# Performance work log

Measured on AMD Instinct MI355X. Metric: run time of the kernel, lower is better.

## Reference

```python
import jax, jax.numpy as jnp
import numpy as np

B, C, H, W = 4, 128, 64, 64
CQ = C // 8  # query/key channels = 16


def setup_inputs() -> dict:
    key = jax.random.key(0)
    ks = jax.random.split(key, 8)
    s = 0.05
    return {
        "x": jax.random.normal(ks[0], (B, C, H, W), jnp.float32),
        "wq": jax.random.normal(ks[1], (CQ, C), jnp.float32) * s,
        "bq": jax.random.normal(ks[2], (CQ,), jnp.float32) * s,
        "wk": jax.random.normal(ks[3], (CQ, C), jnp.float32) * s,
        "bk": jax.random.normal(ks[4], (CQ,), jnp.float32) * s,
        "wv": jax.random.normal(ks[5], (C, C), jnp.float32) * s,
        "bv": jax.random.normal(ks[6], (C,), jnp.float32) * s,
        # original inits gamma to 0; use small nonzero so attention path is exercised
        "gamma": jax.random.normal(ks[7], (1,), jnp.float32) * 0.1,
    }


def reference(x, wq, bq, wk, bk, wv, bv, gamma):
    b, c, h, w = x.shape
    n = h * w
    xf = x.reshape(b, c, n)  # [B, C, N]
    # 1x1 convs are per-position linear maps over channels
    q = jnp.einsum("qc,bcn->bnq", wq, xf) + bq            # [B, N, Cq]
    k = jnp.einsum("qc,bcn->bqn", wk, xf) + bk[:, None]   # [B, Cq, N]
    v = jnp.einsum("oc,bcn->bon", wv, xf) + bv[:, None]   # [B, C, N]
    # unscaled scores, softmax over keys (last dim), as in the original
    attn = jax.nn.softmax(jnp.einsum("bnq,bqm->bnm", q, k), axis=-1)  # [B, N, N]
    # out = value @ attention^T : out[b,c,n] = sum_m v[b,c,m] * attn[b,n,m]
    out = jnp.einsum("bom,bnm->bon", v, attn)             # [B, C, N]
    return gamma[0] * out.reshape(b, c, h, w) + x
```

## Files before the change

kernel.cpp:

```cpp
#include <hip/hip_runtime.h>
#include <hip/hip_bf16.h>

typedef float f32x4  __attribute__((ext_vector_type(4)));
typedef float f32x16 __attribute__((ext_vector_type(16)));
typedef short s16x8  __attribute__((ext_vector_type(8)));
typedef unsigned int u32;

#define NB 4
#define NC 128
#define NNPOS 4096
#define KSP 6
#define LOG2E 1.44269504088896f

__device__ __forceinline__ short bf16s(float x) {
    __hip_bfloat16 h = __float2bfloat16(x);
    return *reinterpret_cast<short*>(&h);
}
__device__ __forceinline__ int packbf2(float lo, float hi) {
    __hip_bfloat162 t = __float22bfloat162_rn(float2{lo, hi});
    return *reinterpret_cast<int*>(&t);
}
__device__ __forceinline__ float bf2f(unsigned short u) {
    unsigned int v = ((unsigned int)u) << 16;
    return *reinterpret_cast<float*>(&v);
}
__device__ __forceinline__ float exp2fast(float x) {
    return __builtin_amdgcn_exp2f(x);
}
__device__ __forceinline__ void gload_lds16(const short* g, short* l) {
    __builtin_amdgcn_global_load_lds(
        (const __attribute__((address_space(1))) u32*)g,
        (__attribute__((address_space(3))) u32*)l, 16, 0, 0);
}

__global__ __launch_bounds__(256) void qkv_kernel(
    const float* __restrict__ x,
    const float* __restrict__ wq, const float* __restrict__ bq,
    const float* __restrict__ wk, const float* __restrict__ bk,
    const float* __restrict__ wv, const float* __restrict__ bv,
    short* __restrict__ qb, short* __restrict__ kb, short* __restrict__ vt)
{
    const int n0  = blockIdx.x * 32;
    const int b   = blockIdx.y;
    const int tid = threadIdx.x;
    const int w = tid >> 6, lane = tid & 63, quad = lane >> 4, nn = lane & 15;

    __shared__ __align__(16) short xsT[32 * 136];
    __shared__ __align__(16) short vstage[4096];

    #pragma unroll
    for (int p = 0; p < 4; ++p) {
        int idx = tid + p * 256;
        int cc = idx >> 3, n4 = (idx & 7) * 4;
        f32x4 xv = *(const f32x4*)&x[((size_t)(b * NC + cc)) * NNPOS + n0 + n4];
        #pragma unroll
        for (int j = 0; j < 4; ++j)
            xsT[(n4 + j) * 136 + cc] = bf16s(xv[j]);
    }

    s16x8 af[3][4];
    bool  live[3];
    f32x4 biasv[3];
    #pragma unroll
    for (int t = 0; t < 3; ++t) {
        int rid = 3 * w + t;
        int R   = rid * 16;
        const float* wsrc = nullptr; const float* bsrc = nullptr; int row0 = 0;
        float scale = 1.0f;
        if (rid < 8)        { wsrc = wv; bsrc = bv; row0 = R; }
        else if (rid == 8)  { wsrc = wq; bsrc = bq; row0 = 0; scale = LOG2E; }
        else if (rid == 10) { wsrc = wk; bsrc = bk; row0 = 0; }
        live[t] = (wsrc != nullptr);
        #pragma unroll
        for (int r = 0; r < 4; ++r)
            biasv[t][r] = live[t] ? scale * bsrc[row0 + quad * 4 + r] : 0.0f;
        if (live[t]) {
            #pragma unroll
            for (int ks = 0; ks < 4; ++ks) {
                const float* src = wsrc + (size_t)(row0 + nn) * NC + ks * 32 + quad * 8;
                f32x4 wa = *(const f32x4*)src;
                f32x4 wb = *(const f32x4*)(src + 4);
                s16x8 f;
                #pragma unroll
                for (int j = 0; j < 4; ++j) {
                    f[j]     = bf16s(scale * wa[j]);
                    f[j + 4] = bf16s(scale * wb[j]);
                }
                af[t][ks] = f;
            }
        }
    }
    __syncthreads();

    f32x4 acc[3][2];
    #pragma unroll
    for (int t = 0; t < 3; ++t)
        #pragma unroll
        for (int nt = 0; nt < 2; ++nt)
            acc[t][nt] = biasv[t];

    #pragma unroll
    for (int nt = 0; nt < 2; ++nt) {
        s16x8 bf[4];
        #pragma unroll
        for (int ks = 0; ks < 4; ++ks)
            bf[ks] = *(const s16x8*)&xsT[(nt * 16 + nn) * 136 + ks * 32 + quad * 8];
        #pragma unroll
        for (int t = 0; t < 3; ++t)
            if (live[t])
                #pragma unroll
                for (int ks = 0; ks < 4; ++ks)
                    acc[t][nt] = __builtin_amdgcn_mfma_f32_16x16x32_bf16(af[t][ks], bf[ks], acc[t][nt], 0, 0, 0);
    }

    const int slot = (nn & 3) | ((nn & 4) << 1) | ((nn & 8) >> 1);

    #pragma unroll
    for (int t = 0; t < 3; ++t) {
        if (!live[t]) continue;
        const int rid = 3 * w + t;
        #pragma unroll
        for (int nt = 0; nt < 2; ++nt) {
            if (rid < 8) {
                #pragma unroll
                for (int r = 0; r < 4; ++r) {
                    int row = rid * 16 + quad * 4 + r;
                    vstage[(((nt << 2) | (row >> 5)) << 9) +
                           ((slot >> 3) << 8) + ((row & 31) << 3) + (slot & 7)]
                        = bf16s(acc[t][nt][r]);
                }
            } else {
                short4 pk;
                pk.x = bf16s(acc[t][nt][0]);
                pk.y = bf16s(acc[t][nt][1]);
                pk.z = bf16s(acc[t][nt][2]);
                pk.w = bf16s(acc[t][nt][3]);
                int n = n0 + nt * 16 + nn;
                short* dst = (rid == 8 ? qb : kb) +
                             ((size_t)(b * NNPOS) + n) * 16 + quad * 4;
                *reinterpret_cast<short4*>(dst) = pk;
            }
        }
    }
    __syncthreads();

    {
        short* vdst = vt + ((size_t)(b * 256) + (n0 >> 4)) * 2048;
        #pragma unroll
        for (int p = 0; p < 2; ++p) {
            int off = (tid + p * 256) * 8;
            *(s16x8*)&vdst[off] = *(const s16x8*)&vstage[off];
        }
    }
}

__global__ __launch_bounds__(256, 3) void attn_kernel(
    const short* __restrict__ qb, const short* __restrict__ kb,
    const short* __restrict__ vt,
    unsigned short* __restrict__ Ow, float* __restrict__ lw)
{
    const int s   = blockIdx.x;
    const int b   = blockIdx.z;
    const int tid = threadIdx.x;
    const int w = tid >> 6, lane = tid & 63, h = lane >> 5, c31 = lane & 31;

    const int q0 = (blockIdx.y * 4 + w) * 32;

    __shared__ __align__(16) short vlds[2][8192];

    s16x8 bq = *(const s16x8*)(qb + ((size_t)(b * NNPOS) + q0 + c31) * 16 + h * 8);

    f32x16 acc[4];
    #pragma unroll
    for (int ct = 0; ct < 4; ++ct)
        #pragma unroll
        for (int r = 0; r < 16; ++r) acc[ct][r] = 0.0f;
    float lp0 = 0.f, lp1 = 0.f;

    const short* kbp = kb + (size_t)(b * NNPOS) * 16;
    const int nit    = (s < 4) ? 11 : 10;
    const int mbase  = (s < 4) ? s * 704 : 2816 + (s - 4) * 640;
    const short* vtile = vt + (size_t)b * (NC * NNPOS) + ((size_t)(mbase >> 4) << 11);

    f32x16 z;
    #pragma unroll
    for (int r = 0; r < 16; ++r) z[r] = 0.0f;

    #pragma unroll
    for (int j = 0; j < 4; ++j)
        gload_lds16(vtile + (tid << 3) + (j << 11),
                    &vlds[0][0] + (tid << 3) + (j << 11));
    int m0 = mbase;
    s16x8 ak0 = *(const s16x8*)(kbp + (size_t)(m0      + c31) * 16 + h * 8);
    s16x8 ak1 = *(const s16x8*)(kbp + (size_t)(m0 + 32 + c31) * 16 + h * 8);
    __syncthreads();

    int buf = 0;
    for (int it = 0; it < nit; ++it) {
        if (it + 1 < nit) {
            const short* src = vtile + (((size_t)(it + 1)) << 13);
            short* dst = &vlds[buf ^ 1][0];
            #pragma unroll
            for (int j = 0; j < 4; ++j)
                gload_lds16(src + (tid << 3) + (j << 11),
                            dst + (tid << 3) + (j << 11));
        }

        f32x16 s0 = __builtin_amdgcn_mfma_f32_32x32x16_bf16(ak0, bq, z, 0, 0, 0);
        f32x16 s1 = __builtin_amdgcn_mfma_f32_32x32x16_bf16(ak1, bq, z, 0, 0, 0);

        if (it + 1 < nit) {
            m0 += 64;
            ak0 = *(const s16x8*)(kbp + (size_t)(m0      + c31) * 16 + h * 8);
            ak1 = *(const s16x8*)(kbp + (size_t)(m0 + 32 + c31) * 16 + h * 8);
        }

        s16x8 pa[4];
        #pragma unroll
        for (int p = 0; p < 4; ++p) {
            const f32x16& sv = (p < 2) ? s0 : s1;
            const int off = (p & 1) * 8;
            union { int i[4]; s16x8 v; } u;
            #pragma unroll
            for (int j = 0; j < 4; ++j) {
                float p0 = exp2fast(sv[off + 2 * j]);
                float p1 = exp2fast(sv[off + 2 * j + 1]);
                if (j & 1) lp1 += p0 + p1; else lp0 += p0 + p1;
                u.i[j] = packbf2(p0, p1);
            }
            pa[p] = u.v;
        }

        const short* vb = &vlds[buf][0];
        #pragma unroll
        for (int p = 0; p < 4; ++p)
            #pragma unroll
            for (int ct = 0; ct < 4; ++ct) {
                s16x8 vf = *(const s16x8*)&vb[((p * 4 + ct) << 9) + (lane << 3)];
                acc[ct] = __builtin_amdgcn_mfma_f32_32x32x16_bf16(
                    pa[p], vf, acc[ct], 0, 0, 0);
            }

        __syncthreads();
        buf ^= 1;
    }

    float lp = lp0 + lp1;
    lp += __shfl_xor(lp, 32, 64);
    if (lane < 32)
        lw[((size_t)(b * KSP + s)) * NNPOS + q0 + c31] = lp;

    #pragma unroll
    for (int ct = 0; ct < 4; ++ct)
        #pragma unroll
        for (int r = 0; r < 16; ++r) {
            int q = q0 + (r & 3) + 8 * (r >> 2) + 4 * h;
            Ow[(((size_t)(b * KSP + s)) * NNPOS + q) * NC + ct * 32 + c31] =
                (unsigned short)bf16s(acc[ct][r]);
        }
}

__global__ __launch_bounds__(256) void combine_kernel(
    const unsigned short* __restrict__ Ow, const float* __restrict__ lw,
    const float* __restrict__ x, const float* __restrict__ gamma,
    float* __restrict__ out)
{
    const int n0  = blockIdx.x * 64;
    const int b   = blockIdx.y;
    const int tid = threadIdx.x;

    __shared__ float ot[128 * 65 + 64];
    float* lsum = ot + 128 * 65;

    if (tid < 64) {
        float sl = 0.f;
        #pragma unroll
        for (int sI = 0; sI < KSP; ++sI)
            sl += lw[((size_t)(b * KSP + sI)) * NNPOS + n0 + tid];
        lsum[tid] = 1.0f / sl;
    }
    __syncthreads();

    #pragma unroll
    for (int p = 0; p < 4; ++p) {
        int e = tid + p * 256;
        int co = e & 15, n = e >> 4;
        float a[8] = {0.f, 0.f, 0.f, 0.f, 0.f, 0.f, 0.f, 0.f};
        #pragma unroll
        for (int sI = 0; sI < KSP; ++sI) {
            const unsigned short* src = Ow +
                (((size_t)(b * KSP + sI)) * NNPOS + n0 + n) * NC + co * 8;
            union { s16x8 v; unsigned short us[8]; } u;
            u.v = *(const s16x8*)src;
            #pragma unroll
            for (int j = 0; j < 8; ++j) a[j] += bf2f(u.us[j]);
        }
        float inv = lsum[n];
        #pragma unroll
        for (int j = 0; j < 8; ++j)
            ot[(co * 8 + j) * 65 + n] = a[j] * inv;
    }
    __syncthreads();

    const float g = gamma[0];
    #pragma unroll
    for (int p = 0; p < 8; ++p) {
        int e = tid + p * 256;
        int nq = e & 15, c = e >> 4;
        size_t a = ((size_t)(b * NC + c)) * NNPOS + n0 + nq * 4;
        float4 xv = *(const float4*)&x[a];
        float4 o;
        o.x = g * ot[c * 65 + nq * 4]     + xv.x;
        o.y = g * ot[c * 65 + nq * 4 + 1] + xv.y;
        o.z = g * ot[c * 65 + nq * 4 + 2] + xv.z;
        o.w = g * ot[c * 65 + nq * 4 + 3] + xv.w;
        *(float4*)&out[a] = o;
    }
}

extern "C" void kernel_launch(void* const* d_in, const int* in_sizes, int n_in,
                              void* d_out, int out_size, void* d_ws, size_t ws_size,
                              hipStream_t stream) {
    const float* x     = (const float*)d_in[0];
    const float* wq    = (const float*)d_in[1];
    const float* bq    = (const float*)d_in[2];
    const float* wk    = (const float*)d_in[3];
    const float* bk    = (const float*)d_in[4];
    const float* wv    = (const float*)d_in[5];
    const float* bv    = (const float*)d_in[6];
    const float* gamma = (const float*)d_in[7];
    float* out = (float*)d_out;

    short* qb = (short*)d_ws;
    short* kb = qb + (size_t)NB * NNPOS * 16;
    short* vt = kb + (size_t)NB * NNPOS * 16;
    unsigned short* Ow = (unsigned short*)(vt + (size_t)NB * NC * NNPOS);
    float* lw = (float*)(Ow + (size_t)NB * KSP * NNPOS * NC);

    qkv_kernel<<<dim3(128, NB), 256, 0, stream>>>(x, wq, bq, wk, bk, wv, bv, qb, kb, vt);
    attn_kernel<<<dim3(KSP, 32, NB), 256, 0, stream>>>(qb, kb, vt, Ow, lw);
    combine_kernel<<<dim3(NNPOS / 64, NB), 256, 0, stream>>>(Ow, lw, x, gamma, out);
}
```

Measured before the change: 114.3 us.

## Process two query tiles per wave to reuse V LDS fragments, split keys eight ways

Each wave now handles 64 queries (two 32-row tiles), so every V fragment read from LDS feeds two MFMAs instead of one. The grid is halved along the query axis, and the key-split count goes from 6 to 8, giving an even 512 keys per split with a fixed trip count. Accumulator registers double and the occupancy hint drops from 3 to 2 blocks per CU. The larger split count also increases the partial-output traffic that combine_kernel must read.

```diff
diff --git a/kernel.cpp b/kernel.cpp
--- a/kernel.cpp
+++ b/kernel.cpp
@@ -9,7 +9,7 @@
 #define NB 4
 #define NC 128
 #define NNPOS 4096
-#define KSP 6
+#define KSP 8
 #define LOG2E 1.44269504088896f
 
 __device__ __forceinline__ short bf16s(float x) {
@@ -154,7 +154,7 @@
     }
 }
 
-__global__ __launch_bounds__(256, 3) void attn_kernel(
+__global__ __launch_bounds__(256, 2) void attn_kernel(
     const short* __restrict__ qb, const short* __restrict__ kb,
     const short* __restrict__ vt,
     unsigned short* __restrict__ Ow, float* __restrict__ lw)
@@ -164,22 +164,24 @@
     const int tid = threadIdx.x;
     const int w = tid >> 6, lane = tid & 63, h = lane >> 5, c31 = lane & 31;
 
-    const int q0 = (blockIdx.y * 4 + w) * 32;
+    const int q0 = (blockIdx.y * 4 + w) * 64;
 
     __shared__ __align__(16) short vlds[2][8192];
 
-    s16x8 bq = *(const s16x8*)(qb + ((size_t)(b * NNPOS) + q0 + c31) * 16 + h * 8);
-
-    f32x16 acc[4];
-    #pragma unroll
-    for (int ct = 0; ct < 4; ++ct)
-        #pragma unroll
-        for (int r = 0; r < 16; ++r) acc[ct][r] = 0.0f;
-    float lp0 = 0.f, lp1 = 0.f;
+    s16x8 bqA = *(const s16x8*)(qb + ((size_t)(b * NNPOS) + q0      + c31) * 16 + h * 8);
+    s16x8 bqB = *(const s16x8*)(qb + ((size_t)(b * NNPOS) + q0 + 32 + c31) * 16 + h * 8);
+
+    f32x16 acc[2][4];
+    #pragma unroll
+    for (int t = 0; t < 2; ++t)
+        #pragma unroll
+        for (int ct = 0; ct < 4; ++ct)
+            #pragma unroll
+            for (int r = 0; r < 16; ++r) acc[t][ct][r] = 0.0f;
+    float lpA0 = 0.f, lpA1 = 0.f, lpB0 = 0.f, lpB1 = 0.f;
 
     const short* kbp = kb + (size_t)(b * NNPOS) * 16;
-    const int nit    = (s < 4) ? 11 : 10;
-    const int mbase  = (s < 4) ? s * 704 : 2816 + (s - 4) * 640;
+    const int mbase  = s * (NNPOS / KSP);
     const short* vtile = vt + (size_t)b * (NC * NNPOS) + ((size_t)(mbase >> 4) << 11);
 
     f32x16 z;
@@ -196,8 +198,9 @@
     __syncthreads();
 
     int buf = 0;
-    for (int it = 0; it < nit; ++it) {
-        if (it + 1 < nit) {
+    #pragma unroll 1
+    for (int it = 0; it < NNPOS / KSP / 64; ++it) {
+        if (it + 1 < NNPOS / KSP / 64) {
             const short* src = vtile + (((size_t)(it + 1)) << 13);
             short* dst = &vlds[buf ^ 1][0];
             #pragma unroll
@@ -206,49 +209,74 @@
                             dst + (tid << 3) + (j << 11));
         }
 
-        f32x16 s0 = __builtin_amdgcn_mfma_f32_32x32x16_bf16(ak0, bq, z, 0, 0, 0);
-        f32x16 s1 = __builtin_amdgcn_mfma_f32_32x32x16_bf16(ak1, bq, z, 0, 0, 0);
-
-        if (it + 1 < nit) {
+        s16x8 paA[4], paB[4];
+        {
+            f32x16 s0 = __builtin_amdgcn_mfma_f32_32x32x16_bf16(ak0, bqA, z, 0, 0, 0);
+            f32x16 s1 = __builtin_amdgcn_mfma_f32_32x32x16_bf16(ak1, bqA, z, 0, 0, 0);
+            #pragma unroll
+            for (int p = 0; p < 4; ++p) {
+                const f32x16& sv = (p < 2) ? s0 : s1;
+                const int off = (p & 1) * 8;
+                union { int i[4]; s16x8 v; } u;
+                #pragma unroll
+                for (int j = 0; j < 4; ++j) {
+                    float p0 = exp2fast(sv[off + 2 * j]);
+                    float p1 = exp2fast(sv[off + 2 * j + 1]);
+                    if (j & 1) lpA1 += p0 + p1; else lpA0 += p0 + p1;
+                    u.i[j] = packbf2(p0, p1);
+                }
+                paA[p] = u.v;
+            }
+        }
+        {
+            f32x16 s0 = __builtin_amdgcn_mfma_f32_32x32x16_bf16(ak0, bqB, z, 0, 0, 0);
+            f32x16 s1 = __builtin_amdgcn_mfma_f32_32x32x16_bf16(ak1, bqB, z, 0, 0, 0);
+            #pragma unroll
+            for (int p = 0; p < 4; ++p) {
+                const f32x16& sv = (p < 2) ? s0 : s1;
+                const int off = (p & 1) * 8;
+                union { int i[4]; s16x8 v; } u;
+                #pragma unroll
+                for (int j = 0; j < 4; ++j) {
+                    float p0 = exp2fast(sv[off + 2 * j]);
+                    float p1 = exp2fast(sv[off + 2 * j + 1]);
+                    if (j & 1) lpB1 += p0 + p1; else lpB0 += p0 + p1;
+                    u.i[j] = packbf2(p0, p1);
+                }
+                paB[p] = u.v;
+            }
+        }
+
+        if (it + 1 < NNPOS / KSP / 64) {
             m0 += 64;
             ak0 = *(const s16x8*)(kbp + (size_t)(m0      + c31) * 16 + h * 8);
             ak1 = *(const s16x8*)(kbp + (size_t)(m0 + 32 + c31) * 16 + h * 8);
         }
 
-        s16x8 pa[4];
-        #pragma unroll
-        for (int p = 0; p < 4; ++p) {
-            const f32x16& sv = (p < 2) ? s0 : s1;
-            const int off = (p & 1) * 8;
-            union { int i[4]; s16x8 v; } u;
-            #pragma unroll
-            for (int j = 0; j < 4; ++j) {
-                float p0 = exp2fast(sv[off + 2 * j]);
-                float p1 = exp2fast(sv[off + 2 * j + 1]);
-                if (j & 1) lp1 += p0 + p1; else lp0 += p0 + p1;
-                u.i[j] = packbf2(p0, p1);
-            }
-            pa[p] = u.v;
-        }
-
         const short* vb = &vlds[buf][0];
         #pragma unroll
         for (int p = 0; p < 4; ++p)
             #pragma unroll
             for (int ct = 0; ct < 4; ++ct) {
                 s16x8 vf = *(const s16x8*)&vb[((p * 4 + ct) << 9) + (lane << 3)];
-                acc[ct] = __builtin_amdgcn_mfma_f32_32x32x16_bf16(
-                    pa[p], vf, acc[ct], 0, 0, 0);
+                acc[0][ct] = __builtin_amdgcn_mfma_f32_32x32x16_bf16(
+                    paA[p], vf, acc[0][ct], 0, 0, 0);
+                acc[1][ct] = __builtin_amdgcn_mfma_f32_32x32x16_bf16(
+                    paB[p], vf, acc[1][ct], 0, 0, 0);
             }
 
         __syncthreads();
         buf ^= 1;
     }
 
-    float lp = lp0 + lp1;
-    lp += __shfl_xor(lp, 32, 64);
-    if (lane < 32)
-        lw[((size_t)(b * KSP + s)) * NNPOS + q0 + c31] = lp;
+    float lpA = lpA0 + lpA1;
+    float lpB = lpB0 + lpB1;
+    lpA += __shfl_xor(lpA, 32, 64);
+    lpB += __shfl_xor(lpB, 32, 64);
+    if (lane < 32) {
+        lw[((size_t)(b * KSP + s)) * NNPOS + q0      + c31] = lpA;
+        lw[((size_t)(b * KSP + s)) * NNPOS + q0 + 32 + c31] = lpB;
+    }
 
     #pragma unroll
     for (int ct = 0; ct < 4; ++ct)
@@ -256,7 +284,9 @@
         for (int r = 0; r < 16; ++r) {
             int q = q0 + (r & 3) + 8 * (r >> 2) + 4 * h;
             Ow[(((size_t)(b * KSP + s)) * NNPOS + q) * NC + ct * 32 + c31] =
-                (unsigned short)bf16s(acc[ct][r]);
+                (unsigned short)bf16s(acc[0][ct][r]);
+            Ow[(((size_t)(b * KSP + s)) * NNPOS + q + 32) * NC + ct * 32 + c31] =
+                (unsigned short)bf16s(acc[1][ct][r]);
         }
 }
 
@@ -338,6 +368,6 @@
     float* lw = (float*)(Ow + (size_t)NB * KSP * NNPOS * NC);
 
     qkv_kernel<<<dim3(128, NB), 256, 0, stream>>>(x, wq, bq, wk, bk, wv, bv, qb, kb, vt);
-    attn_kernel<<<dim3(KSP, 32, NB), 256, 0, stream>>>(qb, kb, vt, Ow, lw);
+    attn_kernel<<<dim3(KSP, 16, NB), 256, 0, stream>>>(qb, kb, vt, Ow, lw);
     combine_kernel<<<dim3(NNPOS / 64, NB), 256, 0, stream>>>(Ow, lw, x, gamma, out);
 }
```

New measurement: 113.1 us. Within noise of the previous version (-1.0%).
